# Kernel optimization log

Hardware: AMD Instinct MI355X
Metric: run time of the kernel (lower is better)

Reference implementation:

```python
import jax, jax.numpy as jnp
import numpy as np

B, T, D, H = 2, 2048, 1024, 16
HD = D // H  # head_size = 64
EPS = 1e-5


def _layernorm(x, g, b):
    mu = jnp.mean(x, axis=-1, keepdims=True)
    var = jnp.mean(jnp.square(x - mu), axis=-1, keepdims=True)
    return (x - mu) * jax.lax.rsqrt(var + EPS) * g + b


def setup_inputs() -> dict:
    key = jax.random.key(0)
    ks = jax.random.split(key, 16)
    s = 0.02
    return {
        "x": jax.random.normal(ks[0], (B, T, D), jnp.float32),
        # per-head Q/K/V linears, stacked over heads: [H, D, HD] (in,out layout)
        "wq": jax.random.normal(ks[1], (H, D, HD), jnp.float32) * s,
        "bq": jnp.zeros((H, HD), jnp.float32),
        "wk": jax.random.normal(ks[2], (H, D, HD), jnp.float32) * s,
        "bk": jnp.zeros((H, HD), jnp.float32),
        "wv": jax.random.normal(ks[3], (H, D, HD), jnp.float32) * s,
        "bv": jnp.zeros((H, HD), jnp.float32),
        "wp": jax.random.normal(ks[4], (D, D), jnp.float32) * s,
        "bp": jnp.zeros((D,), jnp.float32),
        "w1": jax.random.normal(ks[5], (D, 4 * D), jnp.float32) * s,
        "b1": jnp.zeros((4 * D,), jnp.float32),
        "w2": jax.random.normal(ks[6], (4 * D, D), jnp.float32) * s,
        "b2": jnp.zeros((D,), jnp.float32),
        "ln1_g": jnp.ones((D,), jnp.float32),
        "ln1_b": jnp.zeros((D,), jnp.float32),
        "lnf_g": jnp.ones((D,), jnp.float32),
        "lnf_b": jnp.zeros((D,), jnp.float32),
        "ln2_g": jnp.ones((D,), jnp.float32),
        "ln2_b": jnp.zeros((D,), jnp.float32),
    }


def reference(x, wq, bq, wk, bk, wv, bv, wp, bp, w1, b1, w2, b2,
              ln1_g, ln1_b, lnf_g, lnf_b, ln2_g, ln2_b):
    b_, t_, d_ = x.shape
    # batched per-head projections: [B,H,T,HD]
    Q = jnp.einsum('btd,hde->bhte', x, wq) + bq[None, :, None, :]
    K = jnp.einsum('btd,hde->bhte', x, wk) + bk[None, :, None, :]
    V = jnp.einsum('btd,hde->bhte', x, wv) + bv[None, :, None, :]
    # raw attention scores, scaled -- NOTE: no softmax, no mask (matches source)
    wei = jnp.einsum('bhte,bhse->bhts', Q, K) * (HD ** -0.5)
    attn = jnp.einsum('bhts,bhse->bhte', wei, V)  # [B,H,T,HD]
    # concat heads along last dim == [B,T,H*HD]
    cat = attn.transpose(0, 2, 1, 3).reshape(b_, t_, d_)
    Kc = K.transpose(0, 2, 1, 3).reshape(b_, t_, d_)
    Vc = V.transpose(0, 2, 1, 3).reshape(b_, t_, d_)
    out = cat @ wp + bp
    out1 = _layernorm(x + out, ln1_g, ln1_b)
    # FeedForward: ln(idx + net(idx)) internally
    ff = jax.nn.relu(out1 @ w1 + b1) @ w2 + b2
    ffo = _layernorm(out1 + ff, lnf_g, lnf_b)
    out2 = _layernorm(out1 + ffo, ln2_g, ln2_b)
    return (out2, Kc, Vc)
```

## Files before the change

### kernel.cpp

```cpp
#include <hip/hip_runtime.h>

typedef unsigned short u16;
typedef __attribute__((ext_vector_type(4))) float f32x4;
typedef __attribute__((ext_vector_type(8))) __bf16 bf16x8;
typedef __attribute__((ext_vector_type(8))) unsigned short u16x8;
typedef __attribute__((ext_vector_type(4))) unsigned short u16x4;

__device__ __forceinline__ u16 f2b(float f) {
    unsigned int u = __builtin_bit_cast(unsigned int, f);
    u = (u + 0x7FFFu + ((u >> 16) & 1u)) >> 16;
    return (u16)u;
}
__device__ __forceinline__ float b2f(u16 h) {
    unsigned int u = ((unsigned int)h) << 16;
    return __builtin_bit_cast(float, u);
}

__device__ __forceinline__ void gload_lds16(const u16* g, u16* l) {
    __builtin_amdgcn_global_load_lds(
        (const __attribute__((address_space(1))) void*)g,
        (__attribute__((address_space(3))) void*)l,
        16, 0, 0);
}

__device__ __forceinline__ bf16x8 lds_frag(const u16* p) {
    u16x8 t = *(const u16x8*)p;
    return __builtin_bit_cast(bf16x8, t);
}

#define FENCE asm volatile("" ::: "memory")
#define BARRIER do { FENCE; __builtin_amdgcn_s_barrier(); FENCE; \
                     __builtin_amdgcn_sched_barrier(0); } while (0)
#define SCHED0 __builtin_amdgcn_sched_barrier(0)
#define LGKM0 do { asm volatile("s_waitcnt lgkmcnt(0)" ::: "memory"); \
                   __builtin_amdgcn_sched_barrier(0); } while (0)
#define WAIT_VM8 do { asm volatile("s_waitcnt vmcnt(8)" ::: "memory"); \
                      __builtin_amdgcn_sched_barrier(0); } while (0)
#define WAIT_VM0 do { asm volatile("s_waitcnt vmcnt(0)" ::: "memory"); \
                      __builtin_amdgcn_sched_barrier(0); } while (0)

__global__ __launch_bounds__(256) void cast_x_kernel(const float* __restrict__ in,
                                                     u16* __restrict__ out) {
    int i = (blockIdx.x * 256 + threadIdx.x) * 4;
    float4 v = *(const float4*)&in[i];
    u16x4 o = { f2b(v.x), f2b(v.y), f2b(v.z), f2b(v.w) };
    *(u16x4*)&out[i] = o;
}

__global__ __launch_bounds__(256) void tr_wqkv(const float* __restrict__ wq,
                                               const float* __restrict__ wk,
                                               const float* __restrict__ wv,
                                               u16* __restrict__ WT) {
    __shared__ float tile[32][33];
    int z = blockIdx.z;
    int sel = z >> 4, h = z & 15;
    const float* w = (sel == 0) ? wq : (sel == 1) ? wk : wv;
    w += (long)h * 65536;
    int tx = threadIdx.x & 31, ty = threadIdx.x >> 5;
    int d0 = blockIdx.x * 32, e0 = blockIdx.y * 32;
#pragma unroll
    for (int i = 0; i < 32; i += 8)
        tile[ty + i][tx] = w[(long)(d0 + ty + i) * 64 + e0 + tx];
    __syncthreads();
#pragma unroll
    for (int i = 0; i < 32; i += 8)
        WT[((long)(sel * 1024 + h * 64 + e0 + ty + i)) * 1024 + d0 + tx] = f2b(tile[tx][ty + i]);
}

__global__ __launch_bounds__(256) void prep_bias(const float* __restrict__ bq,
                                                 const float* __restrict__ bk,
                                                 const float* __restrict__ bv,
                                                 float* __restrict__ BI) {
    int i = blockIdx.x * 256 + threadIdx.x;
    const float* b = (i < 1024) ? bq : (i < 2048) ? bk : bv;
    BI[i] = b[((i & 1023) >> 6) * 64 + (i & 63)];
}

__global__ __launch_bounds__(256) void transpose_cast(const float* __restrict__ in,
                                                      u16* __restrict__ out, int R, int C) {
    __shared__ float tile[32][33];
    int tx = threadIdx.x & 31, ty = threadIdx.x >> 5;
    int r0 = blockIdx.y * 32, c0 = blockIdx.x * 32;
#pragma unroll
    for (int i = 0; i < 32; i += 8)
        tile[ty + i][tx] = in[(long)(r0 + ty + i) * C + c0 + tx];
    __syncthreads();
#pragma unroll
    for (int i = 0; i < 32; i += 8)
        out[(long)(c0 + ty + i) * R + r0 + tx] = f2b(tile[tx][ty + i]);
}

__global__ __launch_bounds__(256) void kv_expand(const u16* __restrict__ QKVB,
                                                 float* __restrict__ kv) {
    int idx = blockIdx.x * 256 + threadIdx.x;
    int row = idx >> 8;
    int co = (idx & 255) * 8;
    u16x8 v = *(const u16x8*)&QKVB[(long)row * 3072 + 1024 + co];
    float4 f0 = { b2f(v[0]), b2f(v[1]), b2f(v[2]), b2f(v[3]) };
    float4 f1 = { b2f(v[4]), b2f(v[5]), b2f(v[6]), b2f(v[7]) };
    long base = (long)(co >> 10) * 4194304 + (long)row * 1024 + (co & 1023);
    *(float4*)&kv[base] = f0;
    *(float4*)&kv[base + 4] = f1;
}

template <int MODE, int WM, int WN, int MF, int NF, bool COLOUT>
__global__ __launch_bounds__(WM * WN * 64, 2) void gemmT(
    const u16* __restrict__ A, const u16* __restrict__ BT, const float* __restrict__ bias,
    u16* __restrict__ Cb, u16* __restrict__ Q0, u16* __restrict__ Q1,
    int M, int N, int K, int lda, int ldb, int ldc, int kchunk) {
    constexpr int T   = WM * WN * 64;
    constexpr int BM  = WM * MF * 16;
    constexpr int BN  = WN * NF * 16;
    constexpr int RPI = T / 8;
    constexpr int LA  = BM / RPI;
    constexpr int LB  = BN / RPI;
    constexpr int EPI = T * 8;
    constexpr int MFH = MF / 2;
    constexpr int ASZ = BM * 64, BSZ = BN * 64;
    __shared__ __align__(16) u16 SMEM[2 * ASZ + 2 * BSZ];
    u16* As0 = SMEM;
    u16* As1 = SMEM + ASZ;
    u16* Bs0 = SMEM + 2 * ASZ;
    u16* Bs1 = SMEM + 2 * ASZ + BSZ;
    const int tid = threadIdx.x;
    const int lane = tid & 63;
    const int wid = tid >> 6;
    const int wr = wid / WN, wc = wid % WN;
    const int ntile = N / BN;
    const int mtile = M / BM;
    int bid = blockIdx.x;
    int kb = 0, ksz = K;
    u16* Pout = Q0;
    if (MODE == 4) {
        int tiles = mtile * ntile;
        int sk = bid / tiles; bid -= sk * tiles;
        kb = sk * kchunk;
        int rem = K - kb; ksz = rem < kchunk ? rem : kchunk;
        Pout = sk ? Q1 : Q0;
    }
    {
        int q = (mtile * ntile) >> 3;
        bid = (bid & 7) * q + (bid >> 3);
    }
    int bi, bj;
    if (COLOUT) { bj = bid / mtile; bi = bid % mtile; }
    else        { bi = bid / ntile; bj = bid % ntile; }
    const int brow = bi * BM, bcol = bj * BN;
    const int nt = ksz >> 6;

    const int srow = tid >> 3;
    const int scol = ((tid & 7) ^ (srow & 7)) << 3;
    const u16* ag = A + (long)(brow + srow) * lda + kb + scol;
    const u16* bg = BT + (long)(bcol + srow) * ldb + kb + scol;
    const long aI = (long)RPI * lda, bI = (long)RPI * ldb;
    const int sdst = tid << 3;

    auto STAGE = [&](u16* lA, u16* lB, int t) {
#pragma unroll
        for (int j = 0; j < LA; ++j)
            gload_lds16(ag + ((long)t << 6) + j * aI, &lA[j * EPI + sdst]);
#pragma unroll
        for (int j = 0; j < LB; ++j)
            gload_lds16(bg + ((long)t << 6) + j * bI, &lB[j * EPI + sdst]);
    };

    f32x4 acc[MF][NF] = {};
    bf16x8 af0[MFH], af1[MFH], bf0[NF], bf1[NF];

    const int ln15 = lane & 15;
    const int eoff = (((lane >> 4) << 3) ^ ((lane & 7) << 3));
    const int arow0 = wr * (MF * 16) + ln15;
    const int brow0 = wc * (NF * 16) + ln15;

#define RD_A(dst, S, kh, mh)                                                   \
    _Pragma("unroll") for (int m4 = 0; m4 < MFH; ++m4)                         \
        dst[m4] = lds_frag(&(S)[((arow0 + (((mh) * MFH + m4) << 4)) << 6) +    \
                                (eoff ^ ((kh) << 5))]);
#define RD_B(dst, S, kh)                                                       \
    _Pragma("unroll") for (int n = 0; n < NF; ++n)                             \
        dst[n] = lds_frag(&(S)[((brow0 + (n << 4)) << 6) + (eoff ^ ((kh) << 5))]);
#define MM(a, b, mh) do {                                                      \
    __builtin_amdgcn_s_setprio(1);                                             \
    _Pragma("unroll") for (int m4 = 0; m4 < MFH; ++m4)                         \
        _Pragma("unroll") for (int n = 0; n < NF; ++n)                         \
            acc[(mh) * MFH + m4][n] = __builtin_amdgcn_mfma_f32_16x16x32_bf16( \
                a[m4], b[n], acc[(mh) * MFH + m4][n], 0, 0, 0);                \
    __builtin_amdgcn_s_setprio(0);                                             \
} while (0)

    STAGE(As0, Bs0, 0);
    if (nt > 1) { STAGE(As1, Bs1, 1); WAIT_VM8; } else { WAIT_VM0; }
    BARRIER;
    RD_B(bf0, Bs0, 0);
    RD_A(af0, As0, 0, 0);

    u16 *Ac = As0, *Bc = Bs0, *Ao = As1, *Bo = Bs1;
    for (int t = 0; t < nt; ++t) {
        const bool hasN = (t + 1 < nt);
        const bool hasNN = (t + 2 < nt);
        RD_A(af1, Ac, 0, 1);
        MM(af0, bf0, 0);
        SCHED0;
        RD_B(bf1, Bc, 1);
        RD_A(af0, Ac, 1, 0);
        MM(af1, bf0, 1);
        SCHED0;
        RD_A(af1, Ac, 1, 1);
        MM(af0, bf1, 0);
        WAIT_VM0;
        BARRIER;
        if (hasN) { RD_B(bf0, Bo, 0); RD_A(af0, Ao, 0, 0); }
        MM(af1, bf1, 1);
        BARRIER;
        if (hasNN) STAGE(Ac, Bc, t + 2);
        SCHED0;
        u16* tp;
        tp = Ac; Ac = Ao; Ao = tp;
        tp = Bc; Bc = Bo; Bo = tp;
    }

    const int crow0 = wr * (MF * 16), ccol0 = wc * (NF * 16);
#pragma unroll
    for (int m = 0; m < MF; ++m) {
        int rbase = crow0 + (m << 4) + ((lane >> 4) << 2);
#pragma unroll
        for (int n = 0; n < NF; ++n) {
            int col = ccol0 + (n << 4) + ln15;
            float bv = (MODE == 4) ? 0.f : bias[bcol + col];
#pragma unroll
            for (int r = 0; r < 4; ++r) {
                float v = acc[m][n][r] + bv;
                if (MODE == 2) v = v > 0.f ? v : 0.f;
                int row = rbase + r;
                SMEM[row * BN + (col ^ ((row & 7) << 3))] = f2b(v);
            }
        }
    }
    LGKM0;
    BARRIER;
    u16* outp = (MODE == 4) ? Pout : Cb;
    constexpr int CHT = BM * BN / 8 / T;
#pragma unroll
    for (int k = 0; k < CHT; ++k) {
        int c = tid + k * T;
        int row = c / (BN / 8), co = (c % (BN / 8)) * 8;
        u16x8 vv = *(const u16x8*)&SMEM[row * BN + (co ^ ((row & 7) << 3))];
        *(u16x8*)&outp[(long)(brow + row) * ldc + bcol + co] = vv;
    }
#undef RD_A
#undef RD_B
#undef MM
}

__global__ __launch_bounds__(256) void ktv_partial(const u16* __restrict__ QKVB,
                                                   float* __restrict__ KTVF) {
    __shared__ __align__(16) u16 Ks[64 * 64];
    __shared__ __align__(16) u16 Vs[64 * 64];
    int tid = threadIdx.x;
    int tc = blockIdx.x, bh = blockIdx.y;
    int b = bh >> 4, h = bh & 15;
    int j = tid & 63, i0 = (tid >> 6) * 16;
    float acc[16] = {};
    for (int st = 0; st < 4; ++st) {
        int t0 = tc * 256 + st * 64;
        __syncthreads();
#pragma unroll
        for (int i = 0; i < 2; ++i) {
            int c = i * 256 + tid;
            long base = (long)(b * 2048 + t0 + (c >> 3)) * 3072 + h * 64 + (c & 7) * 8;
            *(u16x8*)&Ks[c * 8] = *(const u16x8*)&QKVB[base + 1024];
            *(u16x8*)&Vs[c * 8] = *(const u16x8*)&QKVB[base + 2048];
        }
        __syncthreads();
        for (int tt = 0; tt < 64; ++tt) {
            float vj = b2f(Vs[tt * 64 + j]);
            u16x8 k0 = *(const u16x8*)&Ks[tt * 64 + i0];
            u16x8 k1 = *(const u16x8*)&Ks[tt * 64 + i0 + 8];
#pragma unroll
            for (int r = 0; r < 8; ++r) acc[r] += b2f(k0[r]) * vj;
#pragma unroll
            for (int r = 0; r < 8; ++r) acc[r + 8] += b2f(k1[r]) * vj;
        }
    }
#pragma unroll
    for (int r = 0; r < 16; ++r)
        atomicAdd(&KTVF[bh * 4096 + (i0 + r) * 64 + j], acc[r]);
}

__global__ __launch_bounds__(256) void cast_ktv(const float* __restrict__ KTVF,
                                                u16* __restrict__ KTVT) {
    int idx = blockIdx.x * 256 + threadIdx.x;
    int bh = idx >> 12, r = idx & 4095;
    int n = r >> 6, k = r & 63;
    KTVT[idx] = f2b(KTVF[bh * 4096 + k * 64 + n] * 0.125f);
}

__global__ __launch_bounds__(256) void attn_gemm(const u16* __restrict__ QKVB,
                                                 const u16* __restrict__ KTVT,
                                                 u16* __restrict__ cat) {
    __shared__ __align__(16) u16 Qs[64 * 64];
    __shared__ __align__(16) u16 Bs[64 * 64];
    int tid = threadIdx.x, wid = tid >> 6, lane = tid & 63;
    int rt = blockIdx.x, bh = blockIdx.y;
    int b = bh >> 4, h = bh & 15;
    long qbase = (long)(b * 2048 + rt * 64) * 3072 + h * 64;
#pragma unroll
    for (int i = 0; i < 2; ++i) {
        int c = i * 256 + tid;
        gload_lds16(QKVB + qbase + (c >> 3) * 3072 + (c & 7) * 8, &Qs[(i * 256 + wid * 64) * 8]);
        gload_lds16(KTVT + bh * 4096 + c * 8, &Bs[(i * 256 + wid * 64) * 8]);
    }
    __syncthreads();
    f32x4 acc[4] = {};
#pragma unroll
    for (int kk = 0; kk < 2; ++kk) {
        bf16x8 a = lds_frag(&Qs[(wid * 16 + (lane & 15)) * 64 + kk * 32 + (lane >> 4) * 8]);
#pragma unroll
        for (int n = 0; n < 4; ++n) {
            bf16x8 bb = lds_frag(&Bs[(n * 16 + (lane & 15)) * 64 + kk * 32 + (lane >> 4) * 8]);
            acc[n] = __builtin_amdgcn_mfma_f32_16x16x32_bf16(a, bb, acc[n], 0, 0, 0);
        }
    }
#pragma unroll
    for (int n = 0; n < 4; ++n)
#pragma unroll
        for (int r = 0; r < 4; ++r) {
            int row = rt * 64 + wid * 16 + (lane >> 4) * 4 + r;
            int col = h * 64 + n * 16 + (lane & 15);
            cat[(long)(b * 2048 + row) * 1024 + col] = f2b(acc[n][r]);
        }
}

__device__ __forceinline__ void block_reduce2(float& a, float& b) {
    __syncthreads();
#pragma unroll
    for (int off = 32; off; off >>= 1) {
        a += __shfl_down(a, off);
        b += __shfl_down(b, off);
    }
    __shared__ float sa[4], sb[4];
    int wid = threadIdx.x >> 6, lane = threadIdx.x & 63;
    if (lane == 0) { sa[wid] = a; sb[wid] = b; }
    __syncthreads();
    a = sa[0] + sa[1] + sa[2] + sa[3];
    b = sb[0] + sb[1] + sb[2] + sb[3];
}

__global__ __launch_bounds__(256) void ln1_kernel(
    const float* __restrict__ x,
    const u16* __restrict__ q0, const u16* __restrict__ q1,
    const float* __restrict__ bp,
    const float* __restrict__ g, const float* __restrict__ bt,
    float* __restrict__ out1f, u16* __restrict__ out1b) {
    int row = blockIdx.x, tid = threadIdx.x;
    long base = (long)row * 1024 + tid * 4;
    float4 xv = *(const float4*)&x[base];
    u16x4 a0 = *(const u16x4*)&q0[base];
    u16x4 a1 = *(const u16x4*)&q1[base];
    float4 bb = *(const float4*)&bp[tid * 4];
    float xa[4] = { xv.x, xv.y, xv.z, xv.w };
    float bba[4] = { bb.x, bb.y, bb.z, bb.w };
    float s[4];
#pragma unroll
    for (int r = 0; r < 4; ++r)
        s[r] = xa[r] + b2f(a0[r]) + b2f(a1[r]) + bba[r];
    float sum = s[0] + s[1] + s[2] + s[3];
    float sq = s[0] * s[0] + s[1] * s[1] + s[2] * s[2] + s[3] * s[3];
    block_reduce2(sum, sq);
    float mu = sum * (1.f / 1024.f);
    float var = sq * (1.f / 1024.f) - mu * mu;
    float rs = rsqrtf(var + 1e-5f);
    float o0 = (s[0] - mu) * rs * g[tid * 4 + 0] + bt[tid * 4 + 0];
    float o1 = (s[1] - mu) * rs * g[tid * 4 + 1] + bt[tid * 4 + 1];
    float o2 = (s[2] - mu) * rs * g[tid * 4 + 2] + bt[tid * 4 + 2];
    float o3 = (s[3] - mu) * rs * g[tid * 4 + 3] + bt[tid * 4 + 3];
    float4 of; of.x = o0; of.y = o1; of.z = o2; of.w = o3;
    u16x4 ob = (u16x4){ f2b(o0), f2b(o1), f2b(o2), f2b(o3) };
    *(float4*)&out1f[base] = of;
    *(u16x4*)&out1b[base] = ob;
}

__global__ __launch_bounds__(256) void lnf_kernel(
    const float* __restrict__ out1f,
    const u16* __restrict__ q0, const u16* __restrict__ q1,
    const float* __restrict__ b2,
    const float* __restrict__ lnfg, const float* __restrict__ lnfb,
    const float* __restrict__ ln2g, const float* __restrict__ ln2b,
    float* __restrict__ out2) {
    int row = blockIdx.x, tid = threadIdx.x;
    long base = (long)row * 1024 + tid * 4;
    float4 o1 = *(const float4*)&out1f[base];
    u16x4 a0 = *(const u16x4*)&q0[base];
    u16x4 a1 = *(const u16x4*)&q1[base];
    float4 bb = *(const float4*)&b2[tid * 4];
    float o1a[4] = { o1.x, o1.y, o1.z, o1.w };
    float bba[4] = { bb.x, bb.y, bb.z, bb.w };
    float s1[4];
#pragma unroll
    for (int r = 0; r < 4; ++r)
        s1[r] = o1a[r] + b2f(a0[r]) + b2f(a1[r]) + bba[r];
    float sum = s1[0] + s1[1] + s1[2] + s1[3];
    float sq = s1[0] * s1[0] + s1[1] * s1[1] + s1[2] * s1[2] + s1[3] * s1[3];
    block_reduce2(sum, sq);
    float mu = sum * (1.f / 1024.f);
    float rs = rsqrtf(sq * (1.f / 1024.f) - mu * mu + 1e-5f);
    float s2[4];
#pragma unroll
    for (int r = 0; r < 4; ++r) {
        float ffo = (s1[r] - mu) * rs * lnfg[tid * 4 + r] + lnfb[tid * 4 + r];
        s2[r] = o1a[r] + ffo;
    }
    float sum2 = s2[0] + s2[1] + s2[2] + s2[3];
    float sq2 = s2[0] * s2[0] + s2[1] * s2[1] + s2[2] * s2[2] + s2[3] * s2[3];
    block_reduce2(sum2, sq2);
    float mu2 = sum2 * (1.f / 1024.f);
    float rs2 = rsqrtf(sq2 * (1.f / 1024.f) - mu2 * mu2 + 1e-5f);
    float4 o;
    o.x = (s2[0] - mu2) * rs2 * ln2g[tid * 4 + 0] + ln2b[tid * 4 + 0];
    o.y = (s2[1] - mu2) * rs2 * ln2g[tid * 4 + 1] + ln2b[tid * 4 + 1];
    o.z = (s2[2] - mu2) * rs2 * ln2g[tid * 4 + 2] + ln2b[tid * 4 + 2];
    o.w = (s2[3] - mu2) * rs2 * ln2g[tid * 4 + 3] + ln2b[tid * 4 + 3];
    *(float4*)&out2[base] = o;
}

extern "C" void kernel_launch(void* const* d_in, const int* in_sizes, int n_in,
                              void* d_out, int out_size, void* d_ws, size_t ws_size,
                              hipStream_t stream) {
    const float* x    = (const float*)d_in[0];
    const float* wq   = (const float*)d_in[1];
    const float* bq   = (const float*)d_in[2];
    const float* wk   = (const float*)d_in[3];
    const float* bk   = (const float*)d_in[4];
    const float* wv   = (const float*)d_in[5];
    const float* bv   = (const float*)d_in[6];
    const float* wp   = (const float*)d_in[7];
    const float* bp   = (const float*)d_in[8];
    const float* w1   = (const float*)d_in[9];
    const float* b1   = (const float*)d_in[10];
    const float* w2   = (const float*)d_in[11];
    const float* b2   = (const float*)d_in[12];
    const float* ln1g = (const float*)d_in[13];
    const float* ln1b = (const float*)d_in[14];
    const float* lnfg = (const float*)d_in[15];
    const float* lnfb = (const float*)d_in[16];
    const float* ln2g = (const float*)d_in[17];
    const float* ln2b = (const float*)d_in[18];

    float* out2 = (float*)d_out;
    float* kv   = (float*)d_out + 4194304;

    char* ws = (char*)d_ws;
    u16*   XB     = (u16*)  (ws + 0);
    u16*   CAT    = XB;
    u16*   WQKVT  = (u16*)  (ws + 8388608);
    float* BQKV   = (float*)(ws + 14680064);
    u16*   WPT    = (u16*)  (ws + 14692352);
    u16*   W1T    = (u16*)  (ws + 16789504);
    u16*   W2T    = (u16*)  (ws + 25178112);
    float* KTVF   = (float*)(ws + 33566720);
    u16*   KTVT   = (u16*)  (ws + 34091008);
    u16*   QKVB   = (u16*)  (ws + 34353152);
    u16*   OUT1B  = QKVB;
    u16*   Q3_0   = (u16*)  (ws + 59518976);
    u16*   Q3_1   = (u16*)  (ws + 67907584);
    float* OUT1F  = (float*)(ws + 76296192);
    u16*   H1     = (u16*)  (ws + 93073408);
    u16*   Q5_0   = (u16*)  (ws + 0);
    u16*   Q5_1   = (u16*)  (ws + 34353152);
    (void)ws_size; (void)in_sizes; (void)n_in; (void)out_size;

    hipMemsetAsync(KTVF, 0, 32 * 4096 * 4, stream);
    cast_x_kernel<<<4096, 256, 0, stream>>>(x, XB);
    tr_wqkv<<<dim3(32, 2, 48), 256, 0, stream>>>(wq, wk, wv, WQKVT);
    prep_bias<<<12, 256, 0, stream>>>(bq, bk, bv, BQKV);
    transpose_cast<<<dim3(32, 32), 256, 0, stream>>>(wp, WPT, 1024, 1024);
    transpose_cast<<<dim3(128, 32), 256, 0, stream>>>(w1, W1T, 1024, 4096);
    transpose_cast<<<dim3(32, 128), 256, 0, stream>>>(w2, W2T, 4096, 1024);

    gemmT<1, 2, 4, 4, 6, true><<<256, 512, 0, stream>>>(
        XB, WQKVT, BQKV, QKVB, nullptr, nullptr,
        4096, 3072, 1024, 1024, 1024, 3072, 0);
    kv_expand<<<4096, 256, 0, stream>>>(QKVB, kv);
    ktv_partial<<<dim3(8, 32), 256, 0, stream>>>(QKVB, KTVF);
    cast_ktv<<<512, 256, 0, stream>>>(KTVF, KTVT);
    attn_gemm<<<dim3(32, 32), 256, 0, stream>>>(QKVB, KTVT, CAT);

    gemmT<4, 2, 2, 4, 4, false><<<512, 256, 0, stream>>>(
        CAT, WPT, nullptr, nullptr, Q3_0, Q3_1,
        4096, 1024, 1024, 1024, 1024, 1024, 512);
    ln1_kernel<<<4096, 256, 0, stream>>>(x, Q3_0, Q3_1, bp, ln1g, ln1b, OUT1F, OUT1B);

    gemmT<2, 2, 4, 8, 4, false><<<256, 512, 0, stream>>>(
        OUT1B, W1T, b1, H1, nullptr, nullptr,
        4096, 4096, 1024, 1024, 1024, 4096, 0);
    gemmT<4, 2, 2, 4, 4, false><<<512, 256, 0, stream>>>(
        H1, W2T, nullptr, nullptr, Q5_0, Q5_1,
        4096, 1024, 4096, 4096, 4096, 1024, 2048);
    lnf_kernel<<<4096, 256, 0, stream>>>(OUT1F, Q5_0, Q5_1, b2,
                                         lnfg, lnfb, ln2g, ln2b, out2);
}
```

Measured before the change: 209.6 us.

## Rewrite GEMM mainloop as triple-buffered K=32 pipeline with split epilogue

Replaces the double-buffered BK=64 GEMM with fine-grained register ping-pong by a three-slot ring of BK=32 LDS stages, prefetching two steps ahead with one barrier per step. This removes the manual sched_barrier/setprio scheduling and halves per-stage LDS footprint. The epilogue is split into two halves when the output tile no longer fits the smaller shared buffer. It trades explicit instruction interleaving for deeper prefetch, and doubles the number of loop iterations and barriers.

```diff
diff --git a/kernel.cpp b/kernel.cpp
--- a/kernel.cpp
+++ b/kernel.cpp
@@ -29,15 +29,9 @@
 }
 
 #define FENCE asm volatile("" ::: "memory")
-#define BARRIER do { FENCE; __builtin_amdgcn_s_barrier(); FENCE; \
-                     __builtin_amdgcn_sched_barrier(0); } while (0)
-#define SCHED0 __builtin_amdgcn_sched_barrier(0)
-#define LGKM0 do { asm volatile("s_waitcnt lgkmcnt(0)" ::: "memory"); \
-                   __builtin_amdgcn_sched_barrier(0); } while (0)
-#define WAIT_VM8 do { asm volatile("s_waitcnt vmcnt(8)" ::: "memory"); \
-                      __builtin_amdgcn_sched_barrier(0); } while (0)
-#define WAIT_VM0 do { asm volatile("s_waitcnt vmcnt(0)" ::: "memory"); \
-                      __builtin_amdgcn_sched_barrier(0); } while (0)
+#define BARRIER do { FENCE; __builtin_amdgcn_s_barrier(); FENCE; } while (0)
+#define WAIT_VM4 asm volatile("s_waitcnt vmcnt(4)" ::: "memory")
+#define WAIT_VM0 asm volatile("s_waitcnt vmcnt(0)" ::: "memory")
 
 __global__ __launch_bounds__(256) void cast_x_kernel(const float* __restrict__ in,
                                                      u16* __restrict__ out) {
@@ -104,24 +98,21 @@
 }
 
 template <int MODE, int WM, int WN, int MF, int NF, bool COLOUT>
-__global__ __launch_bounds__(WM * WN * 64, 2) void gemmT(
+__global__ __launch_bounds__(WM * WN * 64, 2) void gemmV(
     const u16* __restrict__ A, const u16* __restrict__ BT, const float* __restrict__ bias,
     u16* __restrict__ Cb, u16* __restrict__ Q0, u16* __restrict__ Q1,
     int M, int N, int K, int lda, int ldb, int ldc, int kchunk) {
     constexpr int T   = WM * WN * 64;
     constexpr int BM  = WM * MF * 16;
     constexpr int BN  = WN * NF * 16;
-    constexpr int RPI = T / 8;
+    constexpr int RPI = T / 4;
     constexpr int LA  = BM / RPI;
     constexpr int LB  = BN / RPI;
     constexpr int EPI = T * 8;
-    constexpr int MFH = MF / 2;
-    constexpr int ASZ = BM * 64, BSZ = BN * 64;
-    __shared__ __align__(16) u16 SMEM[2 * ASZ + 2 * BSZ];
-    u16* As0 = SMEM;
-    u16* As1 = SMEM + ASZ;
-    u16* Bs0 = SMEM + 2 * ASZ;
-    u16* Bs1 = SMEM + 2 * ASZ + BSZ;
+    constexpr int SLOT = (BM + BN) * 32;
+    constexpr int EPH = (BM * BN > 3 * SLOT) ? 2 : 1;
+    constexpr int HR  = BM / EPH;
+    __shared__ __align__(16) u16 SMEM[3 * SLOT];
     const int tid = threadIdx.x;
     const int lane = tid & 63;
     const int wid = tid >> 6;
@@ -146,110 +137,89 @@
     if (COLOUT) { bj = bid / mtile; bi = bid % mtile; }
     else        { bi = bid / ntile; bj = bid % ntile; }
     const int brow = bi * BM, bcol = bj * BN;
-    const int nt = ksz >> 6;
-
-    const int srow = tid >> 3;
-    const int scol = ((tid & 7) ^ (srow & 7)) << 3;
+    const int nt = ksz >> 5;
+
+    const int srow = tid >> 2;
+    const int scol = ((tid & 3) ^ (srow & 3)) << 3;
     const u16* ag = A + (long)(brow + srow) * lda + kb + scol;
     const u16* bg = BT + (long)(bcol + srow) * ldb + kb + scol;
     const long aI = (long)RPI * lda, bI = (long)RPI * ldb;
     const int sdst = tid << 3;
 
-    auto STAGE = [&](u16* lA, u16* lB, int t) {
+    auto STG = [&](u16* s, int t) {
 #pragma unroll
         for (int j = 0; j < LA; ++j)
-            gload_lds16(ag + ((long)t << 6) + j * aI, &lA[j * EPI + sdst]);
+            gload_lds16(ag + ((long)t << 5) + j * aI, &s[j * EPI + sdst]);
 #pragma unroll
         for (int j = 0; j < LB; ++j)
-            gload_lds16(bg + ((long)t << 6) + j * bI, &lB[j * EPI + sdst]);
+            gload_lds16(bg + ((long)t << 5) + j * bI, &s[LA * EPI + j * EPI + sdst]);
     };
 
     f32x4 acc[MF][NF] = {};
-    bf16x8 af0[MFH], af1[MFH], bf0[NF], bf1[NF];
 
     const int ln15 = lane & 15;
-    const int eoff = (((lane >> 4) << 3) ^ ((lane & 7) << 3));
+    const int eoff = (((lane >> 4) << 3) ^ ((lane & 3) << 3));
     const int arow0 = wr * (MF * 16) + ln15;
     const int brow0 = wc * (NF * 16) + ln15;
 
-#define RD_A(dst, S, kh, mh)                                                   \
-    _Pragma("unroll") for (int m4 = 0; m4 < MFH; ++m4)                         \
-        dst[m4] = lds_frag(&(S)[((arow0 + (((mh) * MFH + m4) << 4)) << 6) +    \
-                                (eoff ^ ((kh) << 5))]);
-#define RD_B(dst, S, kh)                                                       \
-    _Pragma("unroll") for (int n = 0; n < NF; ++n)                             \
-        dst[n] = lds_frag(&(S)[((brow0 + (n << 4)) << 6) + (eoff ^ ((kh) << 5))]);
-#define MM(a, b, mh) do {                                                      \
-    __builtin_amdgcn_s_setprio(1);                                             \
-    _Pragma("unroll") for (int m4 = 0; m4 < MFH; ++m4)                         \
-        _Pragma("unroll") for (int n = 0; n < NF; ++n)                         \
-            acc[(mh) * MFH + m4][n] = __builtin_amdgcn_mfma_f32_16x16x32_bf16( \
-                a[m4], b[n], acc[(mh) * MFH + m4][n], 0, 0, 0);                \
-    __builtin_amdgcn_s_setprio(0);                                             \
-} while (0)
-
-    STAGE(As0, Bs0, 0);
-    if (nt > 1) { STAGE(As1, Bs1, 1); WAIT_VM8; } else { WAIT_VM0; }
+    u16 *p0 = SMEM, *p1 = SMEM + SLOT, *p2 = SMEM + 2 * SLOT;
+    STG(p0, 0);
+    STG(p1, 1);
+    WAIT_VM4;
     BARRIER;
-    RD_B(bf0, Bs0, 0);
-    RD_A(af0, As0, 0, 0);
-
-    u16 *Ac = As0, *Bc = Bs0, *Ao = As1, *Bo = Bs1;
+
     for (int t = 0; t < nt; ++t) {
-        const bool hasN = (t + 1 < nt);
-        const bool hasNN = (t + 2 < nt);
-        RD_A(af1, Ac, 0, 1);
-        MM(af0, bf0, 0);
-        SCHED0;
-        RD_B(bf1, Bc, 1);
-        RD_A(af0, Ac, 1, 0);
-        MM(af1, bf0, 1);
-        SCHED0;
-        RD_A(af1, Ac, 1, 1);
-        MM(af0, bf1, 0);
-        WAIT_VM0;
+        if (t + 2 < nt) STG(p2, t + 2);
+        bf16x8 bf[NF], af[MF];
+#pragma unroll
+        for (int n = 0; n < NF; ++n)
+            bf[n] = lds_frag(&p0[BM * 32 + (brow0 + (n << 4)) * 32 + eoff]);
+#pragma unroll
+        for (int m = 0; m < MF; ++m)
+            af[m] = lds_frag(&p0[(arow0 + (m << 4)) * 32 + eoff]);
+#pragma unroll
+        for (int m = 0; m < MF; ++m)
+#pragma unroll
+            for (int n = 0; n < NF; ++n)
+                acc[m][n] = __builtin_amdgcn_mfma_f32_16x16x32_bf16(af[m], bf[n], acc[m][n], 0, 0, 0);
+        if (t + 2 < nt) { WAIT_VM4; } else { WAIT_VM0; }
         BARRIER;
-        if (hasN) { RD_B(bf0, Bo, 0); RD_A(af0, Ao, 0, 0); }
-        MM(af1, bf1, 1);
-        BARRIER;
-        if (hasNN) STAGE(Ac, Bc, t + 2);
-        SCHED0;
-        u16* tp;
-        tp = Ac; Ac = Ao; Ao = tp;
-        tp = Bc; Bc = Bo; Bo = tp;
-    }
-
-    const int crow0 = wr * (MF * 16), ccol0 = wc * (NF * 16);
-#pragma unroll
-    for (int m = 0; m < MF; ++m) {
-        int rbase = crow0 + (m << 4) + ((lane >> 4) << 2);
-#pragma unroll
-        for (int n = 0; n < NF; ++n) {
-            int col = ccol0 + (n << 4) + ln15;
-            float bv = (MODE == 4) ? 0.f : bias[bcol + col];
-#pragma unroll
-            for (int r = 0; r < 4; ++r) {
-                float v = acc[m][n][r] + bv;
-                if (MODE == 2) v = v > 0.f ? v : 0.f;
-                int row = rbase + r;
-                SMEM[row * BN + (col ^ ((row & 7) << 3))] = f2b(v);
+        u16* tp = p0; p0 = p1; p1 = p2; p2 = tp;
+    }
+
+    u16* outp = (MODE == 4) ? Pout : Cb;
+    const int ccol0 = wc * (NF * 16);
+    const int crow0 = wr * (MF * 16);
+    for (int h = 0; h < EPH; ++h) {
+        if (EPH == 1 || wr == h) {
+#pragma unroll
+            for (int m = 0; m < MF; ++m) {
+                int rb = (EPH == 1 ? crow0 : 0) + (m << 4) + ((lane >> 4) << 2);
+#pragma unroll
+                for (int n = 0; n < NF; ++n) {
+                    int col = ccol0 + (n << 4) + ln15;
+                    float bv = (MODE == 4) ? 0.f : bias[bcol + col];
+#pragma unroll
+                    for (int r = 0; r < 4; ++r) {
+                        float v = acc[m][n][r] + bv;
+                        if (MODE == 2) v = v > 0.f ? v : 0.f;
+                        int row = rb + r;
+                        SMEM[row * BN + (col ^ ((row & 3) << 3))] = f2b(v);
+                    }
+                }
             }
         }
-    }
-    LGKM0;
-    BARRIER;
-    u16* outp = (MODE == 4) ? Pout : Cb;
-    constexpr int CHT = BM * BN / 8 / T;
-#pragma unroll
-    for (int k = 0; k < CHT; ++k) {
-        int c = tid + k * T;
-        int row = c / (BN / 8), co = (c % (BN / 8)) * 8;
-        u16x8 vv = *(const u16x8*)&SMEM[row * BN + (co ^ ((row & 7) << 3))];
-        *(u16x8*)&outp[(long)(brow + row) * ldc + bcol + co] = vv;
-    }
-#undef RD_A
-#undef RD_B
-#undef MM
+        __syncthreads();
+        constexpr int CHT = HR * BN / 8 / T;
+#pragma unroll
+        for (int k2 = 0; k2 < CHT; ++k2) {
+            int c = tid + k2 * T;
+            int row = c / (BN / 8), co = (c % (BN / 8)) * 8;
+            u16x8 vv = *(const u16x8*)&SMEM[row * BN + (co ^ ((row & 3) << 3))];
+            *(u16x8*)&outp[(long)(brow + h * HR + row) * ldc + bcol + co] = vv;
+        }
+        if (EPH == 2 && h == 0) __syncthreads();
+    }
 }
 
 __global__ __launch_bounds__(256) void ktv_partial(const u16* __restrict__ QKVB,
@@ -477,7 +447,7 @@
     transpose_cast<<<dim3(128, 32), 256, 0, stream>>>(w1, W1T, 1024, 4096);
     transpose_cast<<<dim3(32, 128), 256, 0, stream>>>(w2, W2T, 4096, 1024);
 
-    gemmT<1, 2, 4, 4, 6, true><<<256, 512, 0, stream>>>(
+    gemmV<1, 2, 4, 4, 6, true><<<256, 512, 0, stream>>>(
         XB, WQKVT, BQKV, QKVB, nullptr, nullptr,
         4096, 3072, 1024, 1024, 1024, 3072, 0);
     kv_expand<<<4096, 256, 0, stream>>>(QKVB, kv);
@@ -485,15 +455,15 @@
     cast_ktv<<<512, 256, 0, stream>>>(KTVF, KTVT);
     attn_gemm<<<dim3(32, 32), 256, 0, stream>>>(QKVB, KTVT, CAT);
 
-    gemmT<4, 2, 2, 4, 4, false><<<512, 256, 0, stream>>>(
+    gemmV<4, 2, 2, 4, 4, false><<<512, 256, 0, stream>>>(
         CAT, WPT, nullptr, nullptr, Q3_0, Q3_1,
         4096, 1024, 1024, 1024, 1024, 1024, 512);
     ln1_kernel<<<4096, 256, 0, stream>>>(x, Q3_0, Q3_1, bp, ln1g, ln1b, OUT1F, OUT1B);
 
-    gemmT<2, 2, 4, 8, 4, false><<<256, 512, 0, stream>>>(
+    gemmV<2, 2, 4, 8, 4, false><<<256, 512, 0, stream>>>(
         OUT1B, W1T, b1, H1, nullptr, nullptr,
         4096, 4096, 1024, 1024, 1024, 4096, 0);
-    gemmT<4, 2, 2, 4, 4, false><<<512, 256, 0, stream>>>(
+    gemmV<4, 2, 2, 4, 4, false><<<512, 256, 0, stream>>>(
         H1, W2T, nullptr, nullptr, Q5_0, Q5_1,
         4096, 1024, 4096, 4096, 4096, 1024, 2048);
     lnf_kernel<<<4096, 256, 0, stream>>>(OUT1F, Q5_0, Q5_1, b2,
```

After: 223.2 us. +6.5%, slower.
